# Kernel optimization log

Measured on AMD Instinct MI355X. Metric: run time of the kernel, lower is better.

Reference implementation:

```python
import jax, jax.numpy as jnp
import numpy as np
import math


def proxy_delta_linear(x, W, gain):
    # x: [B,T,Din], W: [Dout,Din], gain: [1,1,Dout]
    D = x.shape[-1]
    xa = jnp.tanh(x)
    wa = jnp.tanh(W)
    x_sq = jnp.sum(xa * xa, axis=-1, keepdims=True)          # [B,T,1]
    w_sq = jnp.sum(wa * wa, axis=-1)                          # [Dout]
    dot = jnp.einsum('btd,od->bto', xa, wa)                   # [B,T,Dout]
    l2_sq = jnp.clip(x_sq + w_sq - 2.0 * dot, 0.0)
    out = 1.0 - l2_sq / D
    return (out - 0.5) * gain


def setup_inputs() -> dict:
    key = jax.random.key(0)
    ks = jax.random.split(key, 6)
    B, T, C = 2, 2048, 1024
    return {
        'x':  jax.random.normal(ks[0], (B, T, C), dtype=jnp.float32),
        'Wq': jax.random.normal(ks[1], (C, C), dtype=jnp.float32) * 0.02,
        'gq': jnp.full((1, 1, C), 2.0, dtype=jnp.float32),
        'Wk': jax.random.normal(ks[2], (C, C), dtype=jnp.float32) * 0.02,
        'gk': jnp.full((1, 1, C), 2.0, dtype=jnp.float32),
        'Wv': jax.random.normal(ks[3], (C, C), dtype=jnp.float32) * 0.02,
        'gv': jnp.full((1, 1, C), 2.0, dtype=jnp.float32),
        'Wo': jax.random.normal(ks[4], (C, C), dtype=jnp.float32) * 0.02,
    }


def reference(x, Wq, gq, Wk, gk, Wv, gv, Wo):
    B, T, C = x.shape
    H = 16
    D = C // H
    scale = math.sqrt(D)
    q = jnp.tanh(proxy_delta_linear(x, Wq, gq)).reshape(B, T, H, D).transpose(0, 2, 1, 3)
    k = jnp.tanh(proxy_delta_linear(x, Wk, gk)).reshape(B, T, H, D).transpose(0, 2, 1, 3)
    v = proxy_delta_linear(x, Wv, gv).reshape(B, T, H, D).transpose(0, 2, 1, 3)
    q_sq = jnp.sum(q * q, axis=-1, keepdims=True)             # [B,H,T,1]
    k_sq = jnp.sum(k * k, axis=-1)[:, :, None, :]             # [B,H,1,T]
    dot = jnp.einsum('bhtd,bhsd->bhts', q, k)                 # [B,H,T,T]
    dist_sq = jnp.clip(q_sq + k_sq - 2.0 * dot, 0.0)
    logits = -dist_sq / (scale * 10.0)
    attn = jax.nn.softmax(logits, axis=-1)
    out = jnp.einsum('bhts,bhsd->bhtd', attn, v)
    out = out.transpose(0, 2, 1, 3).reshape(B, T, C)
    return jnp.einsum('btc,oc->bto', out, Wo)
```

## Files before the change

kernel.cpp:

```cpp
#include <hip/hip_runtime.h>
#include <hip/hip_bf16.h>
#include <math.h>

typedef unsigned short u16;
typedef unsigned int u32;
typedef __attribute__((ext_vector_type(8))) short short8;
typedef __attribute__((ext_vector_type(8))) unsigned short ushort8;
typedef __attribute__((ext_vector_type(4))) float floatx4;
typedef __attribute__((ext_vector_type(2))) unsigned int uint2v;

#define CDIM   1024
#define TSEQ   2048
#define NHEAD  16
#define HDIM   64

static __device__ __forceinline__ u16 f2bf(float f) {
    u32 u = __float_as_uint(f);
    u += 0x7fffu + ((u >> 16) & 1u);
    return (u16)(u >> 16);
}

static __device__ __forceinline__ u32 cvtpk(float a, float b) {
    u32 r;
    asm("v_cvt_pk_bf16_f32 %0, %1, %2" : "=v"(r) : "v"(a), "v"(b));
    return r;
}

static __device__ __forceinline__ float ftanh(float x) {
    float e = exp2f(x * 2.88539008f);
    float r = __builtin_amdgcn_rcpf(e + 1.0f);
    return fmaf(-2.0f, r, 1.0f);
}

static __device__ __forceinline__ void gll16(const void* g, void* l) {
    __builtin_amdgcn_global_load_lds(
        (const __attribute__((address_space(1))) unsigned int*)g,
        (__attribute__((address_space(3))) unsigned int*)l, 16, 0, 0);
}

__global__ __launch_bounds__(256) void prep(const float* __restrict__ x,
                                            const float* __restrict__ Wq, const float* __restrict__ Wk,
                                            const float* __restrict__ Wv, const float* __restrict__ Wo,
                                            u16* __restrict__ xa,
                                            u16* __restrict__ waq, u16* __restrict__ wak,
                                            u16* __restrict__ wav, u16* __restrict__ wob,
                                            float* __restrict__ xsq,
                                            float* __restrict__ sqq, float* __restrict__ sqk,
                                            float* __restrict__ sqv) {
    __shared__ float red[4];
    int bid = blockIdx.x, tid = threadIdx.x;
    const float* src; u16* dst; float* sq; int row; bool do_tanh = true;
    if (bid < 4096) {
        row = bid; src = x; dst = xa; sq = xsq;
    } else {
        int mat = (bid - 4096) >> 10; row = (bid - 4096) & 1023;
        src = (mat == 0) ? Wq : (mat == 1) ? Wk : (mat == 2) ? Wv : Wo;
        dst = (mat == 0) ? waq : (mat == 1) ? wak : (mat == 2) ? wav : wob;
        sq  = (mat == 0) ? sqq : (mat == 1) ? sqk : (mat == 2) ? sqv : nullptr;
        do_tanh = (mat < 3);
    }
    float4 v = reinterpret_cast<const float4*>(src + (size_t)row * CDIM)[tid];
    if (do_tanh) {
        float a0 = ftanh(v.x), a1 = ftanh(v.y), a2 = ftanh(v.z), a3 = ftanh(v.w);
        *reinterpret_cast<ushort4*>(dst + (size_t)row * CDIM + tid * 4) =
            make_ushort4(f2bf(a0), f2bf(a1), f2bf(a2), f2bf(a3));
        float s = a0*a0 + a1*a1 + a2*a2 + a3*a3;
        #pragma unroll
        for (int m = 1; m < 64; m <<= 1) s += __shfl_xor(s, m, 64);
        if ((tid & 63) == 0) red[tid >> 6] = s;
        __syncthreads();
        if (tid == 0 && sq) sq[row] = red[0] + red[1] + red[2] + red[3];
    } else {
        *reinterpret_cast<ushort4*>(dst + (size_t)row * CDIM + tid * 4) =
            make_ushort4(f2bf(v.x), f2bf(v.y), f2bf(v.z), f2bf(v.w));
    }
}

__global__ __launch_bounds__(256) void gemm_qkv(const u16* __restrict__ xa,
                                                const u16* __restrict__ waq, const u16* __restrict__ wak, const u16* __restrict__ wav,
                                                u16* __restrict__ qb, u16* __restrict__ kb, u16* __restrict__ vT,
                                                const float* __restrict__ xsq,
                                                const float* __restrict__ sqq, const float* __restrict__ sqk, const float* __restrict__ sqv,
                                                const float* __restrict__ gq, const float* __restrict__ gk, const float* __restrict__ gv,
                                                float* __restrict__ qsqT, float* __restrict__ ksqT) {
    __shared__ __align__(16) u16 As[128 * 64];
    __shared__ __align__(16) u16 Bs[128 * 64];
    int z = blockIdx.z;
    const u16* Bm   = (z == 0) ? waq : (z == 1) ? wak : wav;
    const float* wsq  = (z == 0) ? sqq : (z == 1) ? sqk : sqv;
    const float* gain = (z == 0) ? gq : (z == 1) ? gk : gv;

    int tid = threadIdx.x;
    int m0 = blockIdx.y * 128, n0 = blockIdx.x * 128;
    int w = tid >> 6, l = tid & 63, wm = w >> 1, wn = w & 1, g = l >> 4, c = l & 15;
    int r8 = l >> 3, sl7 = l & 7;
    int cmask = (c & 7) ^ (c >> 3);

    floatx4 acc[4][4] = {};

    for (int kt = 0; kt < 16; ++kt) {
        __syncthreads();
        #pragma unroll
        for (int i = 0; i < 4; i++) {
            int ch = w * 4 + i;
            int row = ch * 8 + r8;
            int sl = sl7 ^ r8 ^ (ch & 1);
            gll16(xa + (size_t)(m0 + row) * CDIM + kt * 64 + sl * 8, &As[ch * 512 + l * 8]);
            gll16(Bm + (size_t)(n0 + row) * CDIM + kt * 64 + sl * 8, &Bs[ch * 512 + l * 8]);
        }
        __syncthreads();
        short8 af[2][4], bf[2][4];
        #pragma unroll
        for (int kk = 0; kk < 2; kk++) {
            #pragma unroll
            for (int mi = 0; mi < 4; mi++)
                af[kk][mi] = *reinterpret_cast<const short8*>(
                    &As[(wm * 64 + mi * 16 + c) * 64 + (((kk * 4 + g) ^ cmask) << 3)]);
            #pragma unroll
            for (int ni = 0; ni < 4; ni++)
                bf[kk][ni] = *reinterpret_cast<const short8*>(
                    &Bs[(wn * 64 + ni * 16 + c) * 64 + (((kk * 4 + g) ^ cmask) << 3)]);
        }
        #pragma unroll
        for (int kk = 0; kk < 2; kk++)
            #pragma unroll
            for (int mi = 0; mi < 4; mi++)
                #pragma unroll
                for (int ni = 0; ni < 4; ni++)
                    acc[mi][ni] = __builtin_amdgcn_mfma_f32_16x16x32_bf16(af[kk][mi], bf[kk][ni], acc[mi][ni], 0, 0, 0);
    }

    if (z < 2) {
        u16* outH = (z == 0) ? qb : kb;
        float* sqo = (z == 0) ? qsqT : ksqT;
        int hh = blockIdx.x * 2 + wn;
        float part[4][4] = {};
        #pragma unroll
        for (int mi = 0; mi < 4; mi++) {
            int rowb = m0 + wm * 64 + mi * 16 + g * 4;
            #pragma unroll
            for (int ni = 0; ni < 4; ni++) {
                int col = n0 + wn * 64 + ni * 16 + c;
                float wsqc = wsq[col], gn = gain[col];
                #pragma unroll
                for (int r = 0; r < 4; r++) {
                    float l2 = fmaxf(xsq[rowb + r] + wsqc - 2.f * acc[mi][ni][r], 0.f);
                    float th = ftanh((0.5f - l2 * (1.f / 1024.f)) * gn);
                    outH[(size_t)(rowb + r) * CDIM + col] = f2bf(th);
                    part[mi][r] += th * th;
                }
            }
        }
        #pragma unroll
        for (int mi = 0; mi < 4; mi++)
            #pragma unroll
            for (int r = 0; r < 4; r++) {
                float s = part[mi][r];
                s += __shfl_xor(s, 1, 64); s += __shfl_xor(s, 2, 64);
                s += __shfl_xor(s, 4, 64); s += __shfl_xor(s, 8, 64);
                if (c == 0) {
                    int row = m0 + wm * 64 + mi * 16 + g * 4 + r;
                    int bb = row >> 11, t = row & 2047;
                    sqo[(size_t)(bb * NHEAD + hh) * TSEQ + t] = s;
                }
            }
    } else {
        #pragma unroll
        for (int mi = 0; mi < 4; mi++) {
            int rowb = m0 + wm * 64 + mi * 16 + g * 4;
            #pragma unroll
            for (int ni = 0; ni < 4; ni++) {
                int col = n0 + wn * 64 + ni * 16 + c;
                float wsqc = wsq[col], gn = gain[col];
                float vals[4];
                #pragma unroll
                for (int r = 0; r < 4; r++) {
                    float l2 = fmaxf(xsq[rowb + r] + wsqc - 2.f * acc[mi][ni][r], 0.f);
                    vals[r] = (0.5f - l2 * (1.f / 1024.f)) * gn;
                }
                int bb = rowb >> 11, t0 = rowb & 2047;
                int hh = col >> 6, dd = col & 63;
                ushort4 pv = make_ushort4(f2bf(vals[0]), f2bf(vals[1]), f2bf(vals[2]), f2bf(vals[3]));
                *reinterpret_cast<ushort4*>(&vT[(((size_t)(bb * NHEAD + hh) * HDIM + dd) << 11) + t0]) = pv;
            }
        }
    }
}

__global__ __launch_bounds__(256) void gemm_out(const u16* __restrict__ A, const u16* __restrict__ Bm,
                                                float* __restrict__ outF) {
    __shared__ __align__(16) u16 As[128 * 64];
    __shared__ __align__(16) u16 Bs[128 * 64];
    int tid = threadIdx.x;
    int m0 = blockIdx.y * 128, n0 = blockIdx.x * 128;
    int w = tid >> 6, l = tid & 63, wm = w >> 1, wn = w & 1, g = l >> 4, c = l & 15;
    int r8 = l >> 3, sl7 = l & 7;
    int cmask = (c & 7) ^ (c >> 3);

    floatx4 acc[4][4] = {};

    for (int kt = 0; kt < 16; ++kt) {
        __syncthreads();
        #pragma unroll
        for (int i = 0; i < 4; i++) {
            int ch = w * 4 + i;
            int row = ch * 8 + r8;
            int sl = sl7 ^ r8 ^ (ch & 1);
            gll16(A + (size_t)(m0 + row) * CDIM + kt * 64 + sl * 8, &As[ch * 512 + l * 8]);
            gll16(Bm + (size_t)(n0 + row) * CDIM + kt * 64 + sl * 8, &Bs[ch * 512 + l * 8]);
        }
        __syncthreads();
        short8 af[2][4], bf[2][4];
        #pragma unroll
        for (int kk = 0; kk < 2; kk++) {
            #pragma unroll
            for (int mi = 0; mi < 4; mi++)
                af[kk][mi] = *reinterpret_cast<const short8*>(
                    &As[(wm * 64 + mi * 16 + c) * 64 + (((kk * 4 + g) ^ cmask) << 3)]);
            #pragma unroll
            for (int ni = 0; ni < 4; ni++)
                bf[kk][ni] = *reinterpret_cast<const short8*>(
                    &Bs[(wn * 64 + ni * 16 + c) * 64 + (((kk * 4 + g) ^ cmask) << 3)]);
        }
        #pragma unroll
        for (int kk = 0; kk < 2; kk++)
            #pragma unroll
            for (int mi = 0; mi < 4; mi++)
                #pragma unroll
                for (int ni = 0; ni < 4; ni++)
                    acc[mi][ni] = __builtin_amdgcn_mfma_f32_16x16x32_bf16(af[kk][mi], bf[kk][ni], acc[mi][ni], 0, 0, 0);
    }

    #pragma unroll
    for (int mi = 0; mi < 4; mi++) {
        int rowb = m0 + wm * 64 + mi * 16 + g * 4;
        #pragma unroll
        for (int ni = 0; ni < 4; ni++) {
            int col = n0 + wn * 64 + ni * 16 + c;
            #pragma unroll
            for (int r = 0; r < 4; r++)
                outF[(size_t)(rowb + r) * CDIM + col] = acc[mi][ni][r];
        }
    }
}

__global__ __launch_bounds__(256) void attn3(const u16* __restrict__ q, const u16* __restrict__ k,
                                             const u16* __restrict__ vT, const float* __restrict__ qsqT,
                                             const float* __restrict__ ksqT, u16* __restrict__ ao) {
    int tt = blockIdx.x, h = blockIdx.y, b = blockIdx.z;
    int tid = threadIdx.x, w = tid >> 6, l = tid & 63, g = l >> 4, c = l & 15;
    int tw = tt * 128 + w * 32;

    __shared__ __align__(16) u16 Ks[2][64 * 64];
    __shared__ __align__(16) u16 Vs[2][64 * 64];
    __shared__ __align__(16) u16 Ps[4][32 * 64];
    __shared__ float lLs[4][2][16];

    const float C2 = -0.018033688f;
    const float M2C2 = 0.036067376f;

    short8 qf[2][2];
    float qsC[2];
    #pragma unroll
    for (int tf = 0; tf < 2; tf++) {
        size_t qrow = (size_t)(b * TSEQ + tw + tf * 16 + c) * CDIM + h * HDIM;
        qf[tf][0] = *reinterpret_cast<const short8*>(&q[qrow + g * 8]);
        qf[tf][1] = *reinterpret_cast<const short8*>(&q[qrow + 32 + g * 8]);
        qsC[tf] = qsqT[(size_t)(b * NHEAD + h) * TSEQ + tw + tf * 16 + c] * C2;
    }
    const float* ksb = ksqT + (size_t)(b * NHEAD + h) * TSEQ;
    const u16* kbase = k + (size_t)(b * TSEQ) * CDIM + h * HDIM;
    const u16* vbase = vT + (size_t)(b * NHEAD + h) * HDIM * TSEQ;

    int r8 = l >> 3, sl7 = l & 7;
    int cmask = (c & 7) ^ (c >> 3);

    floatx4 oacc[2][4] = {};
    float lrun[2] = {0.f, 0.f};

    #pragma unroll
    for (int i = 0; i < 2; i++) {
        int ch = w * 2 + i;
        int sl = sl7 ^ r8 ^ (ch & 1);
        gll16(kbase + (size_t)(ch * 8 + r8) * CDIM + sl * 8, &Ks[0][ch * 512 + l * 8]);
        gll16(vbase + (size_t)(ch * 8 + r8) * TSEQ + sl * 8, &Vs[0][ch * 512 + l * 8]);
    }
    __syncthreads();

    for (int st = 0; st < 32; ++st) {
        int cur = st & 1;
        if (st < 31) {
            int s1 = (st + 1) * 64;
            #pragma unroll
            for (int i = 0; i < 2; i++) {
                int ch = w * 2 + i;
                int sl = sl7 ^ r8 ^ (ch & 1);
                gll16(kbase + (size_t)(s1 + ch * 8 + r8) * CDIM + sl * 8, &Ks[cur ^ 1][ch * 512 + l * 8]);
                gll16(vbase + (size_t)(ch * 8 + r8) * TSEQ + s1 + sl * 8, &Vs[cur ^ 1][ch * 512 + l * 8]);
            }
        }

        short8 kf[4][2];
        #pragma unroll
        for (int si = 0; si < 4; si++)
            #pragma unroll
            for (int kc = 0; kc < 2; kc++)
                kf[si][kc] = *reinterpret_cast<const short8*>(
                    &Ks[cur][(si * 16 + c) * 64 + (((kc * 4 + g) ^ cmask) << 3)]);
        floatx4 sacc[2][4] = {};
        #pragma unroll
        for (int tf = 0; tf < 2; tf++)
            #pragma unroll
            for (int si = 0; si < 4; si++) {
                sacc[tf][si] = __builtin_amdgcn_mfma_f32_16x16x32_bf16(kf[si][0], qf[tf][0], sacc[tf][si], 0, 0, 0);
                sacc[tf][si] = __builtin_amdgcn_mfma_f32_16x16x32_bf16(kf[si][1], qf[tf][1], sacc[tf][si], 0, 0, 0);
            }

        float4 kq[4];
        #pragma unroll
        for (int si = 0; si < 4; si++)
            kq[si] = *reinterpret_cast<const float4*>(&ksb[st * 64 + si * 16 + g * 4]);

        #pragma unroll
        for (int tf = 0; tf < 2; tf++) {
            float psum = 0.f;
            #pragma unroll
            for (int si = 0; si < 4; si++) {
                float kqa[4] = {kq[si].x, kq[si].y, kq[si].z, kq[si].w};
                float p[4];
                #pragma unroll
                for (int r = 0; r < 4; r++) {
                    float arg = fmaf(sacc[tf][si][r], M2C2, fmaf(kqa[r], C2, qsC[tf]));
                    p[r] = exp2f(fminf(arg, 0.f));
                    psum += p[r];
                }
                u32 w0 = cvtpk(p[0], p[1]), w1 = cvtpk(p[2], p[3]);
                int pg = ((si * 2 + (g >> 1)) ^ cmask);
                uint2v pw = {w0, w1};
                *reinterpret_cast<uint2v*>(&Ps[w][(tf * 16 + c) * 64 + pg * 8 + (g & 1) * 4]) = pw;
            }
            psum += __shfl_xor(psum, 16, 64);
            psum += __shfl_xor(psum, 32, 64);
            lrun[tf] += psum;
        }

        short8 pa[2][2];
        #pragma unroll
        for (int tf = 0; tf < 2; tf++)
            #pragma unroll
            for (int sc = 0; sc < 2; sc++)
                pa[tf][sc] = *reinterpret_cast<const short8*>(
                    &Ps[w][(tf * 16 + c) * 64 + (((sc * 4 + g) ^ cmask) << 3)]);
        #pragma unroll
        for (int di = 0; di < 4; di++)
            #pragma unroll
            for (int sc = 0; sc < 2; sc++) {
                short8 vf = *reinterpret_cast<const short8*>(
                    &Vs[cur][(di * 16 + c) * 64 + (((sc * 4 + g) ^ cmask) << 3)]);
                #pragma unroll
                for (int tf = 0; tf < 2; tf++)
                    oacc[tf][di] = __builtin_amdgcn_mfma_f32_16x16x32_bf16(pa[tf][sc], vf, oacc[tf][di], 0, 0, 0);
            }

        __syncthreads();
    }

    if (g == 0) { lLs[w][0][c] = lrun[0]; lLs[w][1][c] = lrun[1]; }
    #pragma unroll
    for (int tf = 0; tf < 2; tf++) {
        float linv[4];
        #pragma unroll
        for (int r = 0; r < 4; r++) linv[r] = __builtin_amdgcn_rcpf(lLs[w][tf][g * 4 + r]);
        #pragma unroll
        for (int di = 0; di < 4; di++)
            #pragma unroll
            for (int r = 0; r < 4; r++)
                ao[(size_t)(b * TSEQ + tw + tf * 16 + g * 4 + r) * CDIM + h * HDIM + di * 16 + c] =
                    f2bf(oacc[tf][di][r] * linv[r]);
    }
}

extern "C" void kernel_launch(void* const* d_in, const int* in_sizes, int n_in,
                              void* d_out, int out_size, void* d_ws, size_t ws_size,
                              hipStream_t stream) {
    const float* x  = (const float*)d_in[0];
    const float* Wq = (const float*)d_in[1];
    const float* gq = (const float*)d_in[2];
    const float* Wk = (const float*)d_in[3];
    const float* gk = (const float*)d_in[4];
    const float* Wv = (const float*)d_in[5];
    const float* gv = (const float*)d_in[6];
    const float* Wo = (const float*)d_in[7];
    float* out = (float*)d_out;

    char* p = (char*)d_ws;
    u16* xa  = (u16*)p;  p += (size_t)8 << 20;
    u16* qb  = (u16*)p;  p += (size_t)8 << 20;
    u16* kb  = (u16*)p;  p += (size_t)8 << 20;
    u16* vT  = (u16*)p;  p += (size_t)8 << 20;
    u16* ao  = (u16*)p;  p += (size_t)8 << 20;
    u16* waq = (u16*)p;  p += (size_t)2 << 20;
    u16* wak = (u16*)p;  p += (size_t)2 << 20;
    u16* wav = (u16*)p;  p += (size_t)2 << 20;
    u16* wob = (u16*)p;  p += (size_t)2 << 20;
    float* xsq  = (float*)p; p += 4096 * 4;
    float* sqq  = (float*)p; p += 1024 * 4;
    float* sqk  = (float*)p; p += 1024 * 4;
    float* sqv  = (float*)p; p += 1024 * 4;
    float* qsqT = (float*)p; p += 4096 * 16 * 4;
    float* ksqT = (float*)p; p += 4096 * 16 * 4;
    (void)ws_size; (void)in_sizes; (void)n_in; (void)out_size;

    prep<<<8192, 256, 0, stream>>>(x, Wq, Wk, Wv, Wo, xa, waq, wak, wav, wob,
                                   xsq, sqq, sqk, sqv);

    dim3 gqkv(8, 32, 3);
    gemm_qkv<<<gqkv, 256, 0, stream>>>(xa, waq, wak, wav, qb, kb, vT, xsq,
                                       sqq, sqk, sqv, gq, gk, gv, qsqT, ksqT);

    dim3 ga(16, NHEAD, 2);
    attn3<<<ga, 256, 0, stream>>>(qb, kb, vT, qsqT, ksqT, ao);

    dim3 gg(8, 32);
    gemm_out<<<gg, 256, 0, stream>>>(ao, wob, out);
}
```

Before: 171.3 us.

## Rewrite attention with 32x32 MFMA, register-resident P and folded q-norm

The attention kernel moves from 16x16x32 to 32x32x16 bf16 MFMA tiles. The probability tile is repacked across lanes with a xor-32 shuffle and fed straight into the PV MFMA, so the LDS write and read-back of P goes away. The per-query squared norm is dropped, since softmax ignores a per-row constant, and the clamp on the exponent argument is removed. The QKV GEMM now writes the key norm pre-scaled by the exponent constant and no longer computes or stores the query norm. The trade-off is larger accumulators and more register pressure, plus slightly different rounding because the distance is no longer clipped at zero.

```diff
diff --git a/kernel.cpp b/kernel.cpp
--- a/kernel.cpp
+++ b/kernel.cpp
@@ -7,12 +7,15 @@
 typedef __attribute__((ext_vector_type(8))) short short8;
 typedef __attribute__((ext_vector_type(8))) unsigned short ushort8;
 typedef __attribute__((ext_vector_type(4))) float floatx4;
-typedef __attribute__((ext_vector_type(2))) unsigned int uint2v;
+typedef __attribute__((ext_vector_type(16))) float floatx16;
 
 #define CDIM   1024
 #define TSEQ   2048
 #define NHEAD  16
 #define HDIM   64
+
+#define C2_CONST  (-0.01803368801111874f)
+#define M2C2_CONST (0.03606737602223748f)
 
 static __device__ __forceinline__ u16 f2bf(float f) {
     u32 u = __float_as_uint(f);
@@ -82,11 +85,11 @@
                                                 const float* __restrict__ xsq,
                                                 const float* __restrict__ sqq, const float* __restrict__ sqk, const float* __restrict__ sqv,
                                                 const float* __restrict__ gq, const float* __restrict__ gk, const float* __restrict__ gv,
-                                                float* __restrict__ qsqT, float* __restrict__ ksqT) {
+                                                float* __restrict__ ksC2T) {
     __shared__ __align__(16) u16 As[128 * 64];
     __shared__ __align__(16) u16 Bs[128 * 64];
     int z = blockIdx.z;
-    const u16* Bm   = (z == 0) ? waq : (z == 1) ? wak : wav;
+    const u16* Bm     = (z == 0) ? waq : (z == 1) ? wak : wav;
     const float* wsq  = (z == 0) ? sqq : (z == 1) ? sqk : sqv;
     const float* gain = (z == 0) ? gq : (z == 1) ? gk : gv;
 
@@ -132,8 +135,6 @@
 
     if (z < 2) {
         u16* outH = (z == 0) ? qb : kb;
-        float* sqo = (z == 0) ? qsqT : ksqT;
-        int hh = blockIdx.x * 2 + wn;
         float part[4][4] = {};
         #pragma unroll
         for (int mi = 0; mi < 4; mi++) {
@@ -151,19 +152,22 @@
                 }
             }
         }
-        #pragma unroll
-        for (int mi = 0; mi < 4; mi++)
-            #pragma unroll
-            for (int r = 0; r < 4; r++) {
-                float s = part[mi][r];
-                s += __shfl_xor(s, 1, 64); s += __shfl_xor(s, 2, 64);
-                s += __shfl_xor(s, 4, 64); s += __shfl_xor(s, 8, 64);
-                if (c == 0) {
-                    int row = m0 + wm * 64 + mi * 16 + g * 4 + r;
-                    int bb = row >> 11, t = row & 2047;
-                    sqo[(size_t)(bb * NHEAD + hh) * TSEQ + t] = s;
+        if (z == 1) {
+            int hh = blockIdx.x * 2 + wn;
+            #pragma unroll
+            for (int mi = 0; mi < 4; mi++)
+                #pragma unroll
+                for (int r = 0; r < 4; r++) {
+                    float s = part[mi][r];
+                    s += __shfl_xor(s, 1, 64); s += __shfl_xor(s, 2, 64);
+                    s += __shfl_xor(s, 4, 64); s += __shfl_xor(s, 8, 64);
+                    if (c == 0) {
+                        int row = m0 + wm * 64 + mi * 16 + g * 4 + r;
+                        int bb = row >> 11, t = row & 2047;
+                        ksC2T[(size_t)(bb * NHEAD + hh) * TSEQ + t] = s * C2_CONST;
+                    }
                 }
-            }
+        }
     } else {
         #pragma unroll
         for (int mi = 0; mi < 4; mi++) {
@@ -244,39 +248,33 @@
     }
 }
 
-__global__ __launch_bounds__(256) void attn3(const u16* __restrict__ q, const u16* __restrict__ k,
-                                             const u16* __restrict__ vT, const float* __restrict__ qsqT,
-                                             const float* __restrict__ ksqT, u16* __restrict__ ao) {
+__global__ __launch_bounds__(256) void attn4(const u16* __restrict__ q, const u16* __restrict__ k,
+                                             const u16* __restrict__ vT,
+                                             const float* __restrict__ ksC2T, u16* __restrict__ ao) {
     int tt = blockIdx.x, h = blockIdx.y, b = blockIdx.z;
-    int tid = threadIdx.x, w = tid >> 6, l = tid & 63, g = l >> 4, c = l & 15;
-    int tw = tt * 128 + w * 32;
+    int tid = threadIdx.x, w = tid >> 6, l = tid & 63;
+    int hi = l >> 5, t32 = l & 31;
+    int twb = tt * 128 + w * 32;
 
     __shared__ __align__(16) u16 Ks[2][64 * 64];
     __shared__ __align__(16) u16 Vs[2][64 * 64];
-    __shared__ __align__(16) u16 Ps[4][32 * 64];
-    __shared__ float lLs[4][2][16];
-
-    const float C2 = -0.018033688f;
-    const float M2C2 = 0.036067376f;
-
-    short8 qf[2][2];
-    float qsC[2];
+    __shared__ __align__(16) float Ls[4][32];
+
+    short8 qf[4];
+    size_t qrow = (size_t)(b * TSEQ + twb + t32) * CDIM + h * HDIM;
     #pragma unroll
-    for (int tf = 0; tf < 2; tf++) {
-        size_t qrow = (size_t)(b * TSEQ + tw + tf * 16 + c) * CDIM + h * HDIM;
-        qf[tf][0] = *reinterpret_cast<const short8*>(&q[qrow + g * 8]);
-        qf[tf][1] = *reinterpret_cast<const short8*>(&q[qrow + 32 + g * 8]);
-        qsC[tf] = qsqT[(size_t)(b * NHEAD + h) * TSEQ + tw + tf * 16 + c] * C2;
-    }
-    const float* ksb = ksqT + (size_t)(b * NHEAD + h) * TSEQ;
+    for (int ks = 0; ks < 4; ks++)
+        qf[ks] = *reinterpret_cast<const short8*>(&q[qrow + ks * 16 + hi * 8]);
+
+    const float* ksb = ksC2T + (size_t)(b * NHEAD + h) * TSEQ;
     const u16* kbase = k + (size_t)(b * TSEQ) * CDIM + h * HDIM;
     const u16* vbase = vT + (size_t)(b * NHEAD + h) * HDIM * TSEQ;
 
     int r8 = l >> 3, sl7 = l & 7;
-    int cmask = (c & 7) ^ (c >> 3);
-
-    floatx4 oacc[2][4] = {};
-    float lrun[2] = {0.f, 0.f};
+    int lmask = (l & 7) ^ ((l >> 3) & 1);
+
+    floatx16 oacc[2] = {};
+    float lrun = 0.f;
 
     #pragma unroll
     for (int i = 0; i < 2; i++) {
@@ -300,84 +298,88 @@
             }
         }
 
-        short8 kf[4][2];
-        #pragma unroll
-        for (int si = 0; si < 4; si++)
-            #pragma unroll
-            for (int kc = 0; kc < 2; kc++)
-                kf[si][kc] = *reinterpret_cast<const short8*>(
-                    &Ks[cur][(si * 16 + c) * 64 + (((kc * 4 + g) ^ cmask) << 3)]);
-        floatx4 sacc[2][4] = {};
-        #pragma unroll
-        for (int tf = 0; tf < 2; tf++)
-            #pragma unroll
-            for (int si = 0; si < 4; si++) {
-                sacc[tf][si] = __builtin_amdgcn_mfma_f32_16x16x32_bf16(kf[si][0], qf[tf][0], sacc[tf][si], 0, 0, 0);
-                sacc[tf][si] = __builtin_amdgcn_mfma_f32_16x16x32_bf16(kf[si][1], qf[tf][1], sacc[tf][si], 0, 0, 0);
-            }
-
-        float4 kq[4];
-        #pragma unroll
-        for (int si = 0; si < 4; si++)
-            kq[si] = *reinterpret_cast<const float4*>(&ksb[st * 64 + si * 16 + g * 4]);
-
-        #pragma unroll
-        for (int tf = 0; tf < 2; tf++) {
-            float psum = 0.f;
-            #pragma unroll
-            for (int si = 0; si < 4; si++) {
-                float kqa[4] = {kq[si].x, kq[si].y, kq[si].z, kq[si].w};
-                float p[4];
-                #pragma unroll
-                for (int r = 0; r < 4; r++) {
-                    float arg = fmaf(sacc[tf][si][r], M2C2, fmaf(kqa[r], C2, qsC[tf]));
-                    p[r] = exp2f(fminf(arg, 0.f));
-                    psum += p[r];
+        u32 pk[2][8];
+        #pragma unroll
+        for (int stile = 0; stile < 2; ++stile) {
+            short8 kf[4];
+            #pragma unroll
+            for (int kstep = 0; kstep < 4; kstep++) {
+                int row = stile * 32 + t32;
+                int slot = (kstep * 2 + hi) ^ lmask;
+                kf[kstep] = *reinterpret_cast<const short8*>(&Ks[cur][row * 64 + slot * 8]);
+            }
+            floatx16 sxx = {};
+            #pragma unroll
+            for (int kstep = 0; kstep < 4; kstep++)
+                sxx = __builtin_amdgcn_mfma_f32_32x32x16_bf16(kf[kstep], qf[kstep], sxx, 0, 0, 0);
+
+            float p[16];
+            #pragma unroll
+            for (int qq = 0; qq < 4; qq++) {
+                float4 kc = *reinterpret_cast<const float4*>(
+                    &ksb[st * 64 + stile * 32 + qq * 8 + hi * 4]);
+                float ka[4] = {kc.x, kc.y, kc.z, kc.w};
+                #pragma unroll
+                for (int j = 0; j < 4; j++) {
+                    float arg = fmaf(sxx[qq * 4 + j], M2C2_CONST, ka[j]);
+                    float pv = exp2f(arg);
+                    p[qq * 4 + j] = pv;
+                    lrun += pv;
                 }
-                u32 w0 = cvtpk(p[0], p[1]), w1 = cvtpk(p[2], p[3]);
-                int pg = ((si * 2 + (g >> 1)) ^ cmask);
-                uint2v pw = {w0, w1};
-                *reinterpret_cast<uint2v*>(&Ps[w][(tf * 16 + c) * 64 + pg * 8 + (g & 1) * 4]) = pw;
-            }
-            psum += __shfl_xor(psum, 16, 64);
-            psum += __shfl_xor(psum, 32, 64);
-            lrun[tf] += psum;
-        }
-
-        short8 pa[2][2];
-        #pragma unroll
-        for (int tf = 0; tf < 2; tf++)
-            #pragma unroll
-            for (int sc = 0; sc < 2; sc++)
-                pa[tf][sc] = *reinterpret_cast<const short8*>(
-                    &Ps[w][(tf * 16 + c) * 64 + (((sc * 4 + g) ^ cmask) << 3)]);
-        #pragma unroll
-        for (int di = 0; di < 4; di++)
-            #pragma unroll
-            for (int sc = 0; sc < 2; sc++) {
-                short8 vf = *reinterpret_cast<const short8*>(
-                    &Vs[cur][(di * 16 + c) * 64 + (((sc * 4 + g) ^ cmask) << 3)]);
-                #pragma unroll
-                for (int tf = 0; tf < 2; tf++)
-                    oacc[tf][di] = __builtin_amdgcn_mfma_f32_16x16x32_bf16(pa[tf][sc], vf, oacc[tf][di], 0, 0, 0);
-            }
-
-        __syncthreads();
-    }
-
-    if (g == 0) { lLs[w][0][c] = lrun[0]; lLs[w][1][c] = lrun[1]; }
+            }
+            #pragma unroll
+            for (int i = 0; i < 8; i++)
+                pk[stile][i] = cvtpk(p[2 * i], p[2 * i + 1]);
+        }
+
+        u32 ex[2][4];
+        #pragma unroll
+        for (int stile = 0; stile < 2; ++stile) {
+            #pragma unroll
+            for (int m = 0; m < 4; m++) {
+                const int p0a[4] = {0, 1, 4, 5};
+                u32 send = hi ? pk[stile][p0a[m]] : pk[stile][p0a[m] + 2];
+                ex[stile][m] = (u32)__shfl_xor((int)send, 32, 64);
+            }
+        }
+
+        #pragma unroll
+        for (int ks = 0; ks < 4; ks++) {
+            int e = ks & 1, stl = ks >> 1;
+            union { u32 u[4]; short8 s; } au;
+            au.u[0] = hi ? ex[stl][2 * e]     : pk[stl][4 * e];
+            au.u[1] = hi ? ex[stl][2 * e + 1] : pk[stl][4 * e + 1];
+            au.u[2] = hi ? pk[stl][4 * e + 2] : ex[stl][2 * e];
+            au.u[3] = hi ? pk[stl][4 * e + 3] : ex[stl][2 * e + 1];
+            short8 af = au.s;
+            #pragma unroll
+            for (int dt = 0; dt < 2; dt++) {
+                int row = dt * 32 + t32;
+                int slot = (ks * 2 + hi) ^ lmask;
+                short8 vf = *reinterpret_cast<const short8*>(&Vs[cur][row * 64 + slot * 8]);
+                oacc[dt] = __builtin_amdgcn_mfma_f32_32x32x16_bf16(af, vf, oacc[dt], 0, 0, 0);
+            }
+        }
+
+        __syncthreads();
+    }
+
+    float ltot = lrun + __shfl_xor(lrun, 32, 64);
+    if (l < 32) Ls[w][l] = ltot;
+    float4 lv[4];
     #pragma unroll
-    for (int tf = 0; tf < 2; tf++) {
-        float linv[4];
-        #pragma unroll
-        for (int r = 0; r < 4; r++) linv[r] = __builtin_amdgcn_rcpf(lLs[w][tf][g * 4 + r]);
-        #pragma unroll
-        for (int di = 0; di < 4; di++)
-            #pragma unroll
-            for (int r = 0; r < 4; r++)
-                ao[(size_t)(b * TSEQ + tw + tf * 16 + g * 4 + r) * CDIM + h * HDIM + di * 16 + c] =
-                    f2bf(oacc[tf][di][r] * linv[r]);
-    }
+    for (int qq = 0; qq < 4; qq++)
+        lv[qq] = *reinterpret_cast<const float4*>(&Ls[w][qq * 8 + hi * 4]);
+    #pragma unroll
+    for (int dt = 0; dt < 2; dt++)
+        #pragma unroll
+        for (int r = 0; r < 16; ++r) {
+            int trow = (r & 3) + 8 * (r >> 2) + 4 * hi;
+            float lval = (r & 3) == 0 ? lv[r >> 2].x : (r & 3) == 1 ? lv[r >> 2].y
+                       : (r & 3) == 2 ? lv[r >> 2].z : lv[r >> 2].w;
+            ao[(size_t)(b * TSEQ + twb + trow) * CDIM + h * HDIM + dt * 32 + t32] =
+                f2bf(oacc[dt][r] * __builtin_amdgcn_rcpf(lval));
+        }
 }
 
 extern "C" void kernel_launch(void* const* d_in, const int* in_sizes, int n_in,
@@ -403,12 +405,11 @@
     u16* wak = (u16*)p;  p += (size_t)2 << 20;
     u16* wav = (u16*)p;  p += (size_t)2 << 20;
     u16* wob = (u16*)p;  p += (size_t)2 << 20;
-    float* xsq  = (float*)p; p += 4096 * 4;
-    float* sqq  = (float*)p; p += 1024 * 4;
-    float* sqk  = (float*)p; p += 1024 * 4;
-    float* sqv  = (float*)p; p += 1024 * 4;
-    float* qsqT = (float*)p; p += 4096 * 16 * 4;
-    float* ksqT = (float*)p; p += 4096 * 16 * 4;
+    float* xsq   = (float*)p; p += 4096 * 4;
+    float* sqq   = (float*)p; p += 1024 * 4;
+    float* sqk   = (float*)p; p += 1024 * 4;
+    float* sqv   = (float*)p; p += 1024 * 4;
+    float* ksC2T = (float*)p; p += 4096 * 16 * 4;
     (void)ws_size; (void)in_sizes; (void)n_in; (void)out_size;
 
     prep<<<8192, 256, 0, stream>>>(x, Wq, Wk, Wv, Wo, xa, waq, wak, wav, wob,
@@ -416,10 +417,10 @@
 
     dim3 gqkv(8, 32, 3);
     gemm_qkv<<<gqkv, 256, 0, stream>>>(xa, waq, wak, wav, qb, kb, vT, xsq,
-                                       sqq, sqk, sqv, gq, gk, gv, qsqT, ksqT);
+                                       sqq, sqk, sqv, gq, gk, gv, ksC2T);
 
     dim3 ga(16, NHEAD, 2);
-    attn3<<<ga, 256, 0, stream>>>(qb, kb, vT, qsqT, ksqT, ao);
+    attn4<<<ga, 256, 0, stream>>>(qb, kb, vT, ksC2T, ao);
 
     dim3 gg(8, 32);
     gemm_out<<<gg, 256, 0, stream>>>(ao, wob, out);
```

Result: slower. 211.8 us (+23.6%).
